# Kernel optimization log

Hardware: AMD Instinct MI355X
Metric: run time of the kernel (lower is better)

The kernel has to match this reference:

```python
import jax, jax.numpy as jnp
import numpy as np

GROUP = 64      # SVDQuant hard-coded group size
QMAX = 7.0      # symmetric int4: values in [-8, 7], scale = max|x| / 7
EPS = 1e-8


def setup_inputs() -> dict:
    key = jax.random.key(0)
    k0, k1, k2, k3, k4 = jax.random.split(key, 5)
    T, K, N, R = 4096, 4096, 4096, 32  # tokens, in_features, out_features, rank

    x = jax.random.normal(k0, (T, K), jnp.float32)

    # Full-precision weight, decomposed offline into low-rank + int4 residual
    w = jax.random.normal(k1, (N, K), jnp.float32) * 0.02
    proj_down = jax.random.normal(k2, (K, R), jnp.float32) * 0.02  # x @ proj_down -> [T, R]
    proj_up = jax.random.normal(k3, (R, N), jnp.float32) * 0.02    # [T, R] @ proj_up -> [T, N]
    residual = w - (proj_down @ proj_up).T  # [N, K]

    # Symmetric per-group int4 quantization of the residual weight
    rg = residual.reshape(N, K // GROUP, GROUP)
    wscales = jnp.maximum(jnp.max(jnp.abs(rg), axis=-1) / QMAX, EPS)  # [N, K/G]
    q_w = jnp.clip(jnp.round(rg / wscales[..., None]), -8, 7).astype(jnp.int8).reshape(N, K)

    smooth = jnp.ones((K,), jnp.float32)  # load_from_replicated sets smooth to ones
    bias = jax.random.normal(k4, (N,), jnp.float32) * 0.02
    return {
        "x": x,
        "q_w": q_w,
        "wscales": wscales,
        "proj_down": proj_down,
        "proj_up": proj_up,
        "smooth": smooth,
        "bias": bias,
    }


def reference(x, q_w, wscales, proj_down, proj_up, smooth, bias):
    T, K = x.shape
    N = q_w.shape[0]

    # smoothing (identity here, per load_from_replicated)
    xs = x * smooth

    # low-rank SVD correction branch (full precision)
    lr = (xs @ proj_down) @ proj_up  # [T, N]

    # W4A4 branch: symmetric per-token per-group int4 activation quantization
    xg = xs.reshape(T, K // GROUP, GROUP)
    ascales = jnp.maximum(jnp.max(jnp.abs(xg), axis=-1) / QMAX, EPS)  # [T, K/G]
    q_x = jnp.clip(jnp.round(xg / ascales[..., None]), -8.0, 7.0)
    x_dq = (q_x * ascales[..., None]).reshape(T, K)  # dequantized activations

    # dequantize int4 weights with per-(out_channel, group) scales
    w_dq = (q_w.astype(jnp.float32).reshape(N, K // GROUP, GROUP)
            * wscales[..., None]).reshape(N, K)

    # fused dequant-matmul + low-rank add + bias
    return lr + x_dq @ w_dq.T + bias
```

## Files before the change

kernel.cpp:

```cpp
#include <hip/hip_runtime.h>
#include <hip/hip_bf16.h>
#include <stdint.h>

#define Tdim 4096
#define Ndim 4096
#define Kdim 4096
#define K2   4160
#define NSPLIT 16

using f32x4  = __attribute__((ext_vector_type(4))) float;
using bf16x8 = __attribute__((ext_vector_type(8))) short;

__device__ inline ushort f2bf(float f) {
  union { float f; unsigned u; } v; v.f = f;
  unsigned lsb = (v.u >> 16) & 1u;
  v.u += 0x7fffu + lsb;
  return (ushort)(v.u >> 16);
}

__device__ inline unsigned pack2(float a, float b) {
  return (unsigned)f2bf(a) | ((unsigned)f2bf(b) << 16);
}

__device__ inline float qd(float v, float s) {
  return fminf(fmaxf(rintf(v / s), -8.f), 7.f) * s;
}

__device__ inline void async16(const void* g, void* l) {
  __builtin_amdgcn_global_load_lds(
      (const __attribute__((address_space(1))) unsigned int*)g,
      (__attribute__((address_space(3))) unsigned int*)l, 16, 0, 0);
}

__global__ __launch_bounds__(256) void prep_pdT_kernel(
    const float* __restrict__ pd, ushort* __restrict__ pdT) {
  const int idx = blockIdx.x * 256 + threadIdx.x;
  const int n = idx >> 12;
  const int k = idx & 4095;
  pdT[(size_t)n * Kdim + k] = f2bf(pd[(size_t)k * 32 + n]);
}

__global__ __launch_bounds__(256) void prep_a_kernel(
    const float* __restrict__ x, const float* __restrict__ smooth,
    const ushort* __restrict__ pdT, ushort* __restrict__ A,
    float* __restrict__ partials) {
  __shared__ __attribute__((aligned(16))) ushort sXS[128 * 136];
  __shared__ __attribute__((aligned(16))) ushort sQ[128 * 136];
  const int tid  = threadIdx.x;
  const int lane = tid & 63;
  const int wave = tid >> 6;
  const int fr  = lane & 15;
  const int fkq = lane >> 4;
  const int fk  = fkq * 8;
  const int tok0 = blockIdx.x * 128;
  const int kc0  = blockIdx.y * 256;
  const int r = tid >> 1;
  const int g = tid & 1;
  const int srow2 = tid >> 2;
  const int scol2 = (tid & 3) * 8;

  f32x4 acc[2][2] = {};

  for (int c = 0; c < 2; ++c) {
    const int kbase = kc0 + c * 128;
    const int kcol  = g * 64;
    const float4* xp = (const float4*)&x[(size_t)(tok0 + r) * Kdim + kbase + kcol];
    const float4* sp = (const float4*)&smooth[kbase + kcol];
    float4 v[16];
#pragma unroll
    for (int q = 0; q < 16; ++q) {
      float4 xv = xp[q], sm = sp[q];
      v[q].x = xv.x * sm.x; v[q].y = xv.y * sm.y;
      v[q].z = xv.z * sm.z; v[q].w = xv.w * sm.w;
    }
    float a = 0.f;
#pragma unroll
    for (int q = 0; q < 16; ++q)
      a = fmaxf(a, fmaxf(fmaxf(fabsf(v[q].x), fabsf(v[q].y)),
                         fmaxf(fabsf(v[q].z), fabsf(v[q].w))));
    const float s = fmaxf(a / 7.0f, 1e-8f);
#pragma unroll
    for (int q2 = 0; q2 < 8; ++q2) {
      const float4 v0 = v[2 * q2], v1 = v[2 * q2 + 1];
      uint4 wx, wq;
      wx.x = pack2(v0.x, v0.y);           wx.y = pack2(v0.z, v0.w);
      wx.z = pack2(v1.x, v1.y);           wx.w = pack2(v1.z, v1.w);
      wq.x = pack2(qd(v0.x, s), qd(v0.y, s)); wq.y = pack2(qd(v0.z, s), qd(v0.w, s));
      wq.z = pack2(qd(v1.x, s), qd(v1.y, s)); wq.w = pack2(qd(v1.z, s), qd(v1.w, s));
      *(uint4*)&sXS[r * 136 + kcol + q2 * 8] = wx;
      *(uint4*)&sQ [r * 136 + kcol + q2 * 8] = wq;
    }
    __syncthreads();

#pragma unroll
    for (int kk = 0; kk < 4; ++kk) {
      const int kglob = kbase + kk * 32 + fk;
      bf16x8 af0 = *(const bf16x8*)&sXS[(wave * 32 + fr) * 136 + kk * 32 + fk];
      bf16x8 af1 = *(const bf16x8*)&sXS[(wave * 32 + 16 + fr) * 136 + kk * 32 + fk];
      bf16x8 b0 = *(const bf16x8*)&pdT[(size_t)fr * Kdim + kglob];
      bf16x8 b1 = *(const bf16x8*)&pdT[(size_t)(16 + fr) * Kdim + kglob];
      acc[0][0] = __builtin_amdgcn_mfma_f32_16x16x32_bf16(af0, b0, acc[0][0], 0, 0, 0);
      acc[0][1] = __builtin_amdgcn_mfma_f32_16x16x32_bf16(af0, b1, acc[0][1], 0, 0, 0);
      acc[1][0] = __builtin_amdgcn_mfma_f32_16x16x32_bf16(af1, b0, acc[1][0], 0, 0, 0);
      acc[1][1] = __builtin_amdgcn_mfma_f32_16x16x32_bf16(af1, b1, acc[1][1], 0, 0, 0);
    }

#pragma unroll
    for (int h = 0; h < 2; ++h) {
      const int rr = srow2 + h * 64;
#pragma unroll
      for (int u = 0; u < 4; ++u)
        *(uint4*)&A[(size_t)(tok0 + rr) * K2 + kbase + scol2 + u * 32] =
            *(const uint4*)&sQ[rr * 136 + scol2 + u * 32];
    }
    __syncthreads();
  }

  float* P = partials + (size_t)blockIdx.y * Tdim * 32;
#pragma unroll
  for (int i = 0; i < 2; ++i) {
    const int row0 = tok0 + wave * 32 + i * 16 + fkq * 4;
#pragma unroll
    for (int j = 0; j < 2; ++j) {
      const int col = j * 16 + fr;
#pragma unroll
      for (int rr = 0; rr < 4; ++rr)
        P[(size_t)(row0 + rr) * 32 + col] = acc[i][j][rr];
    }
  }
}

__global__ __launch_bounds__(256) void wprep_kernel(
    const int* __restrict__ qw, const float* __restrict__ wsc,
    const float* __restrict__ partials, const float* __restrict__ pu,
    ushort* __restrict__ A, ushort* __restrict__ B) {
  const int bid = blockIdx.x;
  if (bid < 8192) {
    const size_t idx = ((size_t)bid * 256 + threadIdx.x) * 8;
    const int n = (int)(idx >> 12);
    const int k = (int)(idx & 4095);
    const float s = wsc[n * 64 + (k >> 6)];
    const int4 q0 = *(const int4*)(qw + idx);
    const int4 q1 = *(const int4*)(qw + idx + 4);
    uint4 o;
    o.x = pack2((float)q0.x * s, (float)q0.y * s);
    o.y = pack2((float)q0.z * s, (float)q0.w * s);
    o.z = pack2((float)q1.x * s, (float)q1.y * s);
    o.w = pack2((float)q1.z * s, (float)q1.w * s);
    *(uint4*)(B + (size_t)n * K2 + k) = o;
  } else if (bid < 8192 + 1024) {
    const int idx = (bid - 8192) * 256 + threadIdx.x;
    const int token = idx >> 6, c = idx & 63;
    ushort v = 0;
    if (c < 32) {
      float s = 0.f;
#pragma unroll
      for (int p = 0; p < NSPLIT; ++p)
        s += partials[(size_t)p * Tdim * 32 + (size_t)token * 32 + c];
      v = f2bf(s);
    }
    A[(size_t)token * K2 + Kdim + c] = v;
  } else {
    const int idx = (bid - 9216) * 256 + threadIdx.x;
    const int n = idx >> 6, c = idx & 63;
    ushort v = 0;
    if (c < 32) v = f2bf(pu[(size_t)c * Ndim + n]);
    B[(size_t)n * K2 + Kdim + c] = v;
  }
}

__global__ __launch_bounds__(256) void gemm_kernel(
    const ushort* __restrict__ A, const ushort* __restrict__ B,
    const float* __restrict__ bias, float* __restrict__ C) {
  __shared__ __attribute__((aligned(16))) ushort sA[2 * 128 * 32];
  __shared__ __attribute__((aligned(16))) ushort sB[2 * 128 * 32];
  const int tid  = threadIdx.x;
  const int lane = tid & 63;
  const int wave = tid >> 6;
  const int wr = (wave >> 1) * 64;
  const int wc = (wave & 1) * 64;
  const int fr = lane & 15;

  const int bid    = blockIdx.y * 32 + blockIdx.x;
  const int super  = bid >> 6;
  const int within = bid & 63;
  const int brow   = (super >> 2) * 8 + (within >> 3);
  const int bcol   = (super & 3) * 8 + (within & 7);
  const size_t arow0 = (size_t)brow * 128;
  const size_t brow0 = (size_t)bcol * 128;

  const int srow = tid >> 2;
  const int cs   = tid & 3;
  const int skc  = (cs ^ ((srow >> 1) & 3)) * 8;
  const int fchunk = (((lane >> 4) ^ ((fr >> 1) & 3))) * 8;

  const ushort* gA = A + (arow0 + srow) * K2 + skc;
  const ushort* gB = B + (brow0 + srow) * K2 + skc;

  f32x4 acc[4][4] = {};

  for (int k0 = 0; k0 < K2; k0 += 64) {
#pragma unroll
    for (int p = 0; p < 2; ++p) {
      async16(gA + p * 32,                   &sA[p * 4096 + tid * 8]);
      async16(gA + p * 32 + (size_t)64 * K2, &sA[p * 4096 + (tid + 256) * 8]);
      async16(gB + p * 32,                   &sB[p * 4096 + tid * 8]);
      async16(gB + p * 32 + (size_t)64 * K2, &sB[p * 4096 + (tid + 256) * 8]);
    }
    gA += 64; gB += 64;
    __syncthreads();

#pragma unroll
    for (int kk = 0; kk < 2; ++kk) {
      bf16x8 af[4], bfr[4];
#pragma unroll
      for (int i = 0; i < 4; ++i)
        af[i] = *(const bf16x8*)&sA[kk * 4096 + (wr + i * 16 + fr) * 32 + fchunk];
#pragma unroll
      for (int j = 0; j < 4; ++j)
        bfr[j] = *(const bf16x8*)&sB[kk * 4096 + (wc + j * 16 + fr) * 32 + fchunk];
#pragma unroll
      for (int i = 0; i < 4; ++i)
#pragma unroll
        for (int j = 0; j < 4; ++j)
          acc[i][j] = __builtin_amdgcn_mfma_f32_16x16x32_bf16(af[i], bfr[j], acc[i][j], 0, 0, 0);
    }
    __syncthreads();
  }

  const int rq = (lane >> 4) * 4;
#pragma unroll
  for (int j = 0; j < 4; ++j) {
    const size_t col = brow0 + wc + j * 16 + fr;
    const float bv = bias[col];
#pragma unroll
    for (int i = 0; i < 4; ++i) {
      const size_t row = arow0 + wr + i * 16 + rq;
#pragma unroll
      for (int r = 0; r < 4; ++r)
        C[(row + r) * Ndim + col] = acc[i][j][r] + bv;
    }
  }
}

extern "C" void kernel_launch(void* const* d_in, const int* in_sizes, int n_in,
                              void* d_out, int out_size, void* d_ws, size_t ws_size,
                              hipStream_t stream) {
  const float* x      = (const float*)d_in[0];
  const int*   qw     = (const int*)d_in[1];
  const float* wsc    = (const float*)d_in[2];
  const float* pd     = (const float*)d_in[3];
  const float* pu     = (const float*)d_in[4];
  const float* smooth = (const float*)d_in[5];
  const float* bias   = (const float*)d_in[6];
  float* out = (float*)d_out;

  const size_t abytes = (size_t)Tdim * K2 * 2;
  ushort* A    = (ushort*)d_ws;
  ushort* B    = (ushort*)((char*)d_ws + abytes);
  ushort* pdT  = (ushort*)((char*)d_ws + 2 * abytes);
  float*  part = (float*)((char*)d_ws + 2 * abytes + 262144);

  hipLaunchKernelGGL(prep_pdT_kernel, dim3(512),    dim3(256), 0, stream, pd, pdT);
  hipLaunchKernelGGL(prep_a_kernel,   dim3(32, NSPLIT), dim3(256), 0, stream, x, smooth, pdT, A, part);
  hipLaunchKernelGGL(wprep_kernel,    dim3(10240),  dim3(256), 0, stream, qw, wsc, part, pu, A, B);
  hipLaunchKernelGGL(gemm_kernel,     dim3(32, 32), dim3(256), 0, stream, A, B, bias, out);
}
```

Measured before the change: 356.0 us.

## Rewrite GEMM with 256x256 tiles, triple-buffered async loads and XCD-aware mapping

```diff
diff --git a/kernel.cpp b/kernel.cpp
--- a/kernel.cpp
+++ b/kernel.cpp
@@ -7,6 +7,7 @@
 #define Kdim 4096
 #define K2   4160
 #define NSPLIT 16
+#define NT   130
 
 using f32x4  = __attribute__((ext_vector_type(4))) float;
 using bf16x8 = __attribute__((ext_vector_type(8))) short;
@@ -169,73 +170,108 @@
   }
 }
 
-__global__ __launch_bounds__(256) void gemm_kernel(
+__global__ __launch_bounds__(512, 2) void gemm_kernel(
     const ushort* __restrict__ A, const ushort* __restrict__ B,
     const float* __restrict__ bias, float* __restrict__ C) {
-  __shared__ __attribute__((aligned(16))) ushort sA[2 * 128 * 32];
-  __shared__ __attribute__((aligned(16))) ushort sB[2 * 128 * 32];
+  __shared__ __attribute__((aligned(16))) ushort sA[3 * 8192];
+  __shared__ __attribute__((aligned(16))) ushort sB[3 * 8192];
   const int tid  = threadIdx.x;
   const int lane = tid & 63;
   const int wave = tid >> 6;
-  const int wr = (wave >> 1) * 64;
-  const int wc = (wave & 1) * 64;
-  const int fr = lane & 15;
-
-  const int bid    = blockIdx.y * 32 + blockIdx.x;
-  const int super  = bid >> 6;
-  const int within = bid & 63;
-  const int brow   = (super >> 2) * 8 + (within >> 3);
-  const int bcol   = (super & 3) * 8 + (within & 7);
-  const size_t arow0 = (size_t)brow * 128;
-  const size_t brow0 = (size_t)bcol * 128;
+  const int wm = wave >> 2;
+  const int wn = wave & 3;
+  const int fr  = lane & 15;
+  const int fkq = lane >> 4;
+  const int fchunk = (fkq ^ ((fr >> 1) & 3)) * 8;
+
+  const int bid  = blockIdx.x;
+  const int xcd  = bid & 7;
+  const int i0   = bid >> 3;
+  const int brow = (xcd >> 1) * 4 + (i0 >> 3);
+  const int bcol = (xcd & 1) * 8 + (i0 & 7);
+  const size_t arow0 = (size_t)brow * 256;
+  const size_t brow0 = (size_t)bcol * 256;
 
   const int srow = tid >> 2;
-  const int cs   = tid & 3;
-  const int skc  = (cs ^ ((srow >> 1) & 3)) * 8;
-  const int fchunk = (((lane >> 4) ^ ((fr >> 1) & 3))) * 8;
-
-  const ushort* gA = A + (arow0 + srow) * K2 + skc;
-  const ushort* gB = B + (brow0 + srow) * K2 + skc;
-
-  f32x4 acc[4][4] = {};
-
-  for (int k0 = 0; k0 < K2; k0 += 64) {
-#pragma unroll
-    for (int p = 0; p < 2; ++p) {
-      async16(gA + p * 32,                   &sA[p * 4096 + tid * 8]);
-      async16(gA + p * 32 + (size_t)64 * K2, &sA[p * 4096 + (tid + 256) * 8]);
-      async16(gB + p * 32,                   &sB[p * 4096 + tid * 8]);
-      async16(gB + p * 32 + (size_t)64 * K2, &sB[p * 4096 + (tid + 256) * 8]);
-    }
-    gA += 64; gB += 64;
-    __syncthreads();
-
-#pragma unroll
-    for (int kk = 0; kk < 2; ++kk) {
-      bf16x8 af[4], bfr[4];
-#pragma unroll
-      for (int i = 0; i < 4; ++i)
-        af[i] = *(const bf16x8*)&sA[kk * 4096 + (wr + i * 16 + fr) * 32 + fchunk];
-#pragma unroll
-      for (int j = 0; j < 4; ++j)
-        bfr[j] = *(const bf16x8*)&sB[kk * 4096 + (wc + j * 16 + fr) * 32 + fchunk];
-#pragma unroll
-      for (int i = 0; i < 4; ++i)
-#pragma unroll
-        for (int j = 0; j < 4; ++j)
-          acc[i][j] = __builtin_amdgcn_mfma_f32_16x16x32_bf16(af[i], bfr[j], acc[i][j], 0, 0, 0);
-    }
-    __syncthreads();
-  }
-
-  const int rq = (lane >> 4) * 4;
+  const int swz  = ((tid & 3) ^ ((tid >> 3) & 3)) * 8;
+  const ushort* gA = A + (arow0 + srow) * K2 + swz;
+  const ushort* gB = B + (brow0 + srow) * K2 + swz;
+
+  const int rbase = wm * 128;
+  const int cbase = wn * 64;
+
+  f32x4 acc[8][4] = {};
+
+#define MF(i, j, a, b) \
+  acc[i][j] = __builtin_amdgcn_mfma_f32_16x16x32_bf16(a, b, acc[i][j], 0, 0, 0)
+#define STAGE_A(st, so) \
+  { async16(gA + (size_t)(st) * 32,                    &sA[(so) + tid * 8]);         \
+    async16(gA + (size_t)(st) * 32 + (size_t)128 * K2, &sA[(so) + (tid + 512) * 8]); }
+#define STAGE_B(st, so) \
+  { async16(gB + (size_t)(st) * 32,                    &sB[(so) + tid * 8]);         \
+    async16(gB + (size_t)(st) * 32 + (size_t)128 * K2, &sB[(so) + (tid + 512) * 8]); }
+#define FENCE() asm volatile("" ::: "memory")
+#define BARRIER() { FENCE(); __builtin_amdgcn_s_barrier(); FENCE(); }
+
+  STAGE_A(0, 0); STAGE_B(0, 0);
+  STAGE_A(1, 8192); STAGE_B(1, 8192);
+  asm volatile("s_waitcnt vmcnt(4)" ::: "memory");
+  BARRIER();
+
+  for (int s = 0; s < NT; ++s) {
+    const int sl  = (s % 3) * 8192;
+    const int sn  = s + 2;
+    const int sln = (sn % 3) * 8192;
+    const ushort* al = &sA[sl];
+    const ushort* bl = &sB[sl];
+
+    bf16x8 af0 = *(const bf16x8*)&al[(rbase +  0 + fr) * 32 + fchunk];
+    bf16x8 af1 = *(const bf16x8*)&al[(rbase + 16 + fr) * 32 + fchunk];
+    bf16x8 af2 = *(const bf16x8*)&al[(rbase + 32 + fr) * 32 + fchunk];
+    bf16x8 af3 = *(const bf16x8*)&al[(rbase + 48 + fr) * 32 + fchunk];
+    bf16x8 bf0 = *(const bf16x8*)&bl[(cbase +  0 + fr) * 32 + fchunk];
+    bf16x8 bf1 = *(const bf16x8*)&bl[(cbase + 16 + fr) * 32 + fchunk];
+    bf16x8 bf2 = *(const bf16x8*)&bl[(cbase + 32 + fr) * 32 + fchunk];
+    bf16x8 bf3 = *(const bf16x8*)&bl[(cbase + 48 + fr) * 32 + fchunk];
+    if (sn < NT) STAGE_A(sn, sln);
+    BARRIER();
+    __builtin_amdgcn_s_setprio(1);
+    MF(0, 0, af0, bf0); MF(1, 0, af1, bf0); MF(2, 0, af2, bf0); MF(3, 0, af3, bf0);
+    MF(0, 1, af0, bf1); MF(1, 1, af1, bf1); MF(2, 1, af2, bf1); MF(3, 1, af3, bf1);
+    MF(0, 2, af0, bf2); MF(1, 2, af1, bf2); MF(2, 2, af2, bf2); MF(3, 2, af3, bf2);
+    MF(0, 3, af0, bf3); MF(1, 3, af1, bf3); MF(2, 3, af2, bf3); MF(3, 3, af3, bf3);
+    __builtin_amdgcn_s_setprio(0);
+    BARRIER();
+
+    af0 = *(const bf16x8*)&al[(rbase +  64 + fr) * 32 + fchunk];
+    af1 = *(const bf16x8*)&al[(rbase +  80 + fr) * 32 + fchunk];
+    af2 = *(const bf16x8*)&al[(rbase +  96 + fr) * 32 + fchunk];
+    af3 = *(const bf16x8*)&al[(rbase + 112 + fr) * 32 + fchunk];
+    if (sn < NT) STAGE_B(sn, sln);
+    BARRIER();
+    __builtin_amdgcn_s_setprio(1);
+    MF(4, 0, af0, bf0); MF(5, 0, af1, bf0); MF(6, 0, af2, bf0); MF(7, 0, af3, bf0);
+    MF(4, 1, af0, bf1); MF(5, 1, af1, bf1); MF(6, 1, af2, bf1); MF(7, 1, af3, bf1);
+    MF(4, 2, af0, bf2); MF(5, 2, af1, bf2); MF(6, 2, af2, bf2); MF(7, 2, af3, bf2);
+    MF(4, 3, af0, bf3); MF(5, 3, af1, bf3); MF(6, 3, af2, bf3); MF(7, 3, af3, bf3);
+    __builtin_amdgcn_s_setprio(0);
+    if (s < NT - 2)       asm volatile("s_waitcnt vmcnt(4)" ::: "memory");
+    else if (s == NT - 2) asm volatile("s_waitcnt vmcnt(0)" ::: "memory");
+    BARRIER();
+  }
+#undef MF
+#undef STAGE_A
+#undef STAGE_B
+#undef FENCE
+#undef BARRIER
+
 #pragma unroll
   for (int j = 0; j < 4; ++j) {
-    const size_t col = brow0 + wc + j * 16 + fr;
+    const size_t col = brow0 + cbase + j * 16 + fr;
     const float bv = bias[col];
 #pragma unroll
-    for (int i = 0; i < 4; ++i) {
-      const size_t row = arow0 + wr + i * 16 + rq;
+    for (int i = 0; i < 8; ++i) {
+      const size_t row = arow0 + rbase + i * 16 + fkq * 4;
 #pragma unroll
       for (int r = 0; r < 4; ++r)
         C[(row + r) * Ndim + col] = acc[i][j][r] + bv;
@@ -264,5 +300,5 @@
   hipLaunchKernelGGL(prep_pdT_kernel, dim3(512),    dim3(256), 0, stream, pd, pdT);
   hipLaunchKernelGGL(prep_a_kernel,   dim3(32, NSPLIT), dim3(256), 0, stream, x, smooth, pdT, A, part);
   hipLaunchKernelGGL(wprep_kernel,    dim3(10240),  dim3(256), 0, stream, qw, wsc, part, pu, A, B);
-  hipLaunchKernelGGL(gemm_kernel,     dim3(32, 32), dim3(256), 0, stream, A, B, bias, out);
-}
+  hipLaunchKernelGGL(gemm_kernel,     dim3(256),    dim3(512), 0, stream, A, B, bias, out);
+}
```

Measured after the change: 328.8 us. -7.6%, faster.

## Enlarge GEMM tile to 128x256 with triple-buffered async pipeline and XCD-aware mapping

Applied to the files above, without the earlier changes.

```diff
diff --git a/kernel.cpp b/kernel.cpp
--- a/kernel.cpp
+++ b/kernel.cpp
@@ -7,6 +7,7 @@
 #define Kdim 4096
 #define K2   4160
 #define NSPLIT 16
+#define NT   130
 
 using f32x4  = __attribute__((ext_vector_type(4))) float;
 using bf16x8 = __attribute__((ext_vector_type(8))) short;
@@ -169,73 +170,101 @@
   }
 }
 
-__global__ __launch_bounds__(256) void gemm_kernel(
+__global__ __launch_bounds__(256, 2) void gemm_kernel(
     const ushort* __restrict__ A, const ushort* __restrict__ B,
     const float* __restrict__ bias, float* __restrict__ C) {
-  __shared__ __attribute__((aligned(16))) ushort sA[2 * 128 * 32];
-  __shared__ __attribute__((aligned(16))) ushort sB[2 * 128 * 32];
+  __shared__ __attribute__((aligned(16))) ushort sA[3 * 4096];
+  __shared__ __attribute__((aligned(16))) ushort sB[3 * 8192];
   const int tid  = threadIdx.x;
   const int lane = tid & 63;
   const int wave = tid >> 6;
-  const int wr = (wave >> 1) * 64;
-  const int wc = (wave & 1) * 64;
-  const int fr = lane & 15;
-
-  const int bid    = blockIdx.y * 32 + blockIdx.x;
-  const int super  = bid >> 6;
-  const int within = bid & 63;
-  const int brow   = (super >> 2) * 8 + (within >> 3);
-  const int bcol   = (super & 3) * 8 + (within & 7);
+  const int wm  = wave >> 1;
+  const int wnn = wave & 1;
+  const int fr  = lane & 15;
+  const int fkq = lane >> 4;
+  const int fchunk = (fkq ^ ((fr >> 1) & 3)) * 8;
+
+  const int bid  = blockIdx.x;
+  const int xcd  = bid & 7;
+  const int i0   = bid >> 3;
+  const int brow = (xcd >> 1) * 8 + (i0 & 7);
+  const int bcol = (xcd & 1) * 8 + (i0 >> 3);
   const size_t arow0 = (size_t)brow * 128;
-  const size_t brow0 = (size_t)bcol * 128;
+  const size_t brow0 = (size_t)bcol * 256;
 
   const int srow = tid >> 2;
-  const int cs   = tid & 3;
-  const int skc  = (cs ^ ((srow >> 1) & 3)) * 8;
-  const int fchunk = (((lane >> 4) ^ ((fr >> 1) & 3))) * 8;
-
-  const ushort* gA = A + (arow0 + srow) * K2 + skc;
-  const ushort* gB = B + (brow0 + srow) * K2 + skc;
-
-  f32x4 acc[4][4] = {};
-
-  for (int k0 = 0; k0 < K2; k0 += 64) {
-#pragma unroll
-    for (int p = 0; p < 2; ++p) {
-      async16(gA + p * 32,                   &sA[p * 4096 + tid * 8]);
-      async16(gA + p * 32 + (size_t)64 * K2, &sA[p * 4096 + (tid + 256) * 8]);
-      async16(gB + p * 32,                   &sB[p * 4096 + tid * 8]);
-      async16(gB + p * 32 + (size_t)64 * K2, &sB[p * 4096 + (tid + 256) * 8]);
-    }
-    gA += 64; gB += 64;
-    __syncthreads();
-
-#pragma unroll
-    for (int kk = 0; kk < 2; ++kk) {
-      bf16x8 af[4], bfr[4];
-#pragma unroll
-      for (int i = 0; i < 4; ++i)
-        af[i] = *(const bf16x8*)&sA[kk * 4096 + (wr + i * 16 + fr) * 32 + fchunk];
-#pragma unroll
-      for (int j = 0; j < 4; ++j)
-        bfr[j] = *(const bf16x8*)&sB[kk * 4096 + (wc + j * 16 + fr) * 32 + fchunk];
-#pragma unroll
-      for (int i = 0; i < 4; ++i)
-#pragma unroll
-        for (int j = 0; j < 4; ++j)
-          acc[i][j] = __builtin_amdgcn_mfma_f32_16x16x32_bf16(af[i], bfr[j], acc[i][j], 0, 0, 0);
-    }
-    __syncthreads();
-  }
-
-  const int rq = (lane >> 4) * 4;
-#pragma unroll
-  for (int j = 0; j < 4; ++j) {
-    const size_t col = brow0 + wc + j * 16 + fr;
+  const int swz  = ((tid & 3) ^ ((srow >> 1) & 3)) * 8;
+  const ushort* gA = A + (arow0 + srow) * K2 + swz;
+  const ushort* gB = B + (brow0 + srow) * K2 + swz;
+
+  const int rbase = wm * 64;
+  const int cbase = wnn * 128;
+
+  f32x4 acc[4][8] = {};
+
+#define SB() __builtin_amdgcn_sched_barrier(0)
+#define STAGE(S, SLA, SLB) do {                                              \
+    const size_t gk_ = (size_t)(S) * 32;                                     \
+    async16(gA + gk_,                     &sA[(SLA) + tid * 8]);             \
+    async16(gA + gk_ + (size_t)64  * K2,  &sA[(SLA) + (tid + 256) * 8]);     \
+    async16(gB + gk_,                     &sB[(SLB) + tid * 8]);             \
+    async16(gB + gk_ + (size_t)64  * K2,  &sB[(SLB) + (tid + 256) * 8]);     \
+    async16(gB + gk_ + (size_t)128 * K2,  &sB[(SLB) + (tid + 512) * 8]);     \
+    async16(gB + gk_ + (size_t)192 * K2,  &sB[(SLB) + (tid + 768) * 8]);     \
+  } while (0)
+
+  STAGE(0, 0, 0);
+  STAGE(1, 4096, 8192);
+  SB();
+  asm volatile("s_waitcnt vmcnt(6)");
+  SB();
+  __builtin_amdgcn_s_barrier();
+  SB();
+
+  int ms = 0, mt = 2;
+  for (int s = 0; s < NT; ++s) {
+    const int slA = ms << 12;
+    const int slB = ms << 13;
+
+    bf16x8 af[4], bfr[8];
+#pragma unroll
+    for (int ii = 0; ii < 4; ++ii)
+      af[ii] = *(const bf16x8*)&sA[slA + (rbase + ii * 16 + fr) * 32 + fchunk];
+#pragma unroll
+    for (int jj = 0; jj < 8; ++jj)
+      bfr[jj] = *(const bf16x8*)&sB[slB + (cbase + jj * 16 + fr) * 32 + fchunk];
+
+    if (s < NT - 2) STAGE(s + 2, mt << 12, mt << 13);
+
+    __builtin_amdgcn_s_setprio(1);
+#pragma unroll
+    for (int jj = 0; jj < 8; ++jj)
+#pragma unroll
+      for (int ii = 0; ii < 4; ++ii)
+        acc[ii][jj] = __builtin_amdgcn_mfma_f32_16x16x32_bf16(
+            af[ii], bfr[jj], acc[ii][jj], 0, 0, 0);
+    __builtin_amdgcn_s_setprio(0);
+
+    SB();
+    if (s < NT - 2)       asm volatile("s_waitcnt vmcnt(6)");
+    else if (s == NT - 2) asm volatile("s_waitcnt vmcnt(0)");
+    SB();
+    __builtin_amdgcn_s_barrier();
+    SB();
+
+    ms = (ms == 2) ? 0 : ms + 1;
+    mt = (mt == 2) ? 0 : mt + 1;
+  }
+#undef SB
+#undef STAGE
+
+#pragma unroll
+  for (int j = 0; j < 8; ++j) {
+    const size_t col = brow0 + cbase + j * 16 + fr;
     const float bv = bias[col];
 #pragma unroll
     for (int i = 0; i < 4; ++i) {
-      const size_t row = arow0 + wr + i * 16 + rq;
+      const size_t row = arow0 + rbase + i * 16 + fkq * 4;
 #pragma unroll
       for (int r = 0; r < 4; ++r)
         C[(row + r) * Ndim + col] = acc[i][j][r] + bv;
@@ -264,5 +293,5 @@
   hipLaunchKernelGGL(prep_pdT_kernel, dim3(512),    dim3(256), 0, stream, pd, pdT);
   hipLaunchKernelGGL(prep_a_kernel,   dim3(32, NSPLIT), dim3(256), 0, stream, x, smooth, pdT, A, part);
   hipLaunchKernelGGL(wprep_kernel,    dim3(10240),  dim3(256), 0, stream, qw, wsc, part, pu, A, B);
-  hipLaunchKernelGGL(gemm_kernel,     dim3(32, 32), dim3(256), 0, stream, A, B, bias, out);
-}
+  hipLaunchKernelGGL(gemm_kernel,     dim3(512),    dim3(256), 0, stream, A, B, bias, out);
+}
```

Result: faster. 326.3 us (-8.3%).
